# Performance work log

Measured on AMD Instinct MI355X. Metric: run time of the kernel, lower is better.

Reference implementation:

```python
import jax, jax.numpy as jnp
import numpy as np
import math

DIMS, HEAD = 1024, 16
HD = DIMS // HEAD          # 64
B, CTX = 4, 1024
MAX_ITER, THRESH = 3, 0.5  # temp=1.0 -> q temperature scaling branch is skipped (as in torch)
LOG10_21 = math.log10(1.0 + 4000.0 / 200.0)


def _freq_angles(c):
    # compute_freqs_base: 0.2*(10**linspace(0, log10(21), d/2) - 1), custom_freqs = 36000/220 * base
    d2 = HD // 2
    mel = 10.0 ** jnp.linspace(0.0, LOG10_21, d2) - 1.0
    freqs = (36000.0 / 220.0) * (200.0 * mel / 1000.0)        # [d2]
    t = jnp.arange(c, dtype=jnp.float32)
    return t[:, None] * freqs[None, :]                          # [c, d2]


def _rope(x, ang):
    # lucidrains rotary_embedding_torch convention: interleaved pairs (x0,x1),(x2,x3),...
    x1, x2 = x[..., 0::2], x[..., 1::2]
    cos, sin = jnp.cos(ang), jnp.sin(ang)
    out = jnp.stack([x1 * cos - x2 * sin, x1 * sin + x2 * cos], axis=-1)
    return out.reshape(x.shape)


def _rms(x, w):
    eps = jnp.finfo(x.dtype).eps  # torch nn.RMSNorm eps=None default
    return x * jax.lax.rsqrt(jnp.mean(jnp.square(x), -1, keepdims=True) + eps) * w


def _sdpa(q, k, v):
    # mask is always None in this module's forward -> non-causal SDPA
    s = jnp.einsum('bhqd,bhkd->bhqk', q, k) / math.sqrt(q.shape[-1])
    return jnp.einsum('bhqk,bhkd->bhqd', jax.nn.softmax(s, -1), v)


def _focus(x, xa, P):
    # x: [b, cq, D] queries, xa: [b, ck, D] keys/values. In our configs cq == ck == eff_span.
    b, cq, D = x.shape
    ck = xa.shape[1]
    q = _rms(x, P['wq_norm']) @ P['Wq'] + P['bq']
    q = q.reshape(b, cq, HEAD, HD).transpose(0, 2, 1, 3)                 # b h c d
    kv = _rms(xa, P['wkv_norm']) @ P['Wkv'] + P['bkv']
    kv = kv.reshape(b, ck, 2, HEAD, HD).transpose(2, 0, 3, 1, 4)         # kv b h c d
    k, v = kv[0], kv[1]
    q = _rope(q, _freq_angles(cq))
    k = _rope(k, _freq_angles(ck))

    e = min(cq, ck)  # static; equals cq in all call sites here
    curq, kc, vc = q, k[:, :, :e], v[:, :, :e]
    prev = jnp.zeros_like(q)
    attn_out = jnp.zeros_like(q)
    done = jnp.asarray(False)
    for it in range(MAX_ITER):
        # torch: q/k/v re-projected from current state EVERY iteration (k,v compound)
        qp = curq[:, :, :e] @ P['Wlq'] + P['blq']
        kp = kc @ P['Wlk'] + P['blk']
        vp = vc @ P['Wlv'] + P['blv']
        attn = _sdpa(_rms(qp, P['wln']), _rms(kp, P['wln']), vp)         # == iter_out since e == cq
        diff = jnp.mean(jnp.abs(attn - prev))
        stop = (diff < THRESH) & (it > 0) & (~done)
        attn_out = jnp.where(done, attn_out, attn)  # on the break iteration attn_out = iter_out
        done = done | stop
        curq = jnp.where(done, curq, curq + attn)
        prev = jnp.where(done, prev, attn)
        kc = jnp.where(done, kc, kp)
        vc = jnp.where(done, vc, vp)
    return attn_out.transpose(0, 2, 1, 3).reshape(b, cq, D)             # b c (h d)


def _slide(x, P):
    # win_size = head_dim; only the first win_size keys of each span are ever used
    b, ctx, D = x.shape
    w = HD
    off = w // HEAD                       # span_len - win_size
    nwin = ctx // w                       # ctx chosen as a multiple of w
    starts = jnp.maximum(jnp.arange(nwin) * w - off, 0)
    kidx = starts[:, None] + jnp.arange(w)[None, :]                      # [nwin, w]
    qwin = x.reshape(b, nwin, w, D).transpose(1, 0, 2, 3)                # [nwin, b, w, D]
    kwin = x[:, kidx, :].transpose(1, 0, 2, 3)                           # [nwin, b, w, D]
    outw = jax.vmap(lambda xq, xk: _focus(xq, xk, P))(qwin, kwin)
    return outw.transpose(1, 0, 2, 3).reshape(b, ctx, D)


def _forward(x, xa, P):
    xw = _slide(x, P)
    xaw = _slide(xa, P)
    out = _focus(xw, xaw, P)
    return out @ P['Wo'] + P['bo']        # Dropout(0.01) is identity in eval


def setup_inputs() -> dict:
    key = jax.random.key(0)
    ks = jax.random.split(key, 8)
    s = 0.02
    f32 = jnp.float32
    return {
        'x': jax.random.normal(ks[0], (B, CTX, DIMS), f32),
        'xa': jax.random.normal(ks[1], (B, CTX, DIMS), f32),
        'wq_norm': jnp.ones((DIMS,), f32),
        'Wq': jax.random.normal(ks[2], (DIMS, DIMS), f32) * s,
        'bq': jnp.zeros((DIMS,), f32),
        'wkv_norm': jnp.ones((DIMS,), f32),
        'Wkv': jax.random.normal(ks[3], (DIMS, 2 * DIMS), f32) * s,
        'bkv': jnp.zeros((2 * DIMS,), f32),
        'wln': jnp.ones((HD,), f32),
        'Wlq': jax.random.normal(ks[4], (HD, HD), f32) * s,
        'blq': jnp.zeros((HD,), f32),
        'Wlk': jax.random.normal(ks[5], (HD, HD), f32) * s,
        'blk': jnp.zeros((HD,), f32),
        'Wlv': jax.random.normal(ks[6], (HD, HD), f32) * s,
        'blv': jnp.zeros((HD,), f32),
        'Wo': jax.random.normal(ks[7], (DIMS, DIMS), f32) * s,
        'bo': jnp.zeros((DIMS,), f32),
    }


def reference(x, xa, wq_norm, Wq, bq, wkv_norm, Wkv, bkv, wln, Wlq, blq, Wlk, blk, Wlv, blv, Wo, bo):
    P = dict(wq_norm=wq_norm, Wq=Wq, bq=bq, wkv_norm=wkv_norm, Wkv=Wkv, bkv=bkv, wln=wln,
             Wlq=Wlq, blq=blq, Wlk=Wlk, blk=blk, Wlv=Wlv, blv=blv, Wo=Wo, bo=bo)
    return _forward(x, xa, P)
```

## Files before the change

### kernel.cpp

```cpp
#include <hip/hip_runtime.h>
#include <math.h>

#define TPB 256

static __device__ __forceinline__ float4 mk4(float a, float b, float c, float d) {
  float4 r; r.x = a; r.y = b; r.z = c; r.w = d; return r;
}

static __device__ __forceinline__ float4 ld4s(const float* buf, int row, int ch) {
  return *(const float4*)&buf[(row << 6) + (((ch ^ (row >> 2)) & 15) << 2)];
}
static __device__ __forceinline__ void st4s(float* buf, int row, int ch, float4 v) {
  *(float4*)&buf[(row << 6) + (((ch ^ (row >> 2)) & 15) << 2)] = v;
}

__global__ __launch_bounds__(TPB) void k_tables(float* __restrict__ cosb,
                                                float* __restrict__ sinb) {
  int gid = blockIdx.x * TPB + threadIdx.x;
  if (gid >= 1024 * 32) return;
  int t = gid >> 5, j = gid & 31;
  const double Ld = 1.3222192947339193;
  float Lf = (float)Ld;
  float mlog;
  if (j == 31) {
    mlog = Lf;
  } else {
    float stepf = (float)((double)j / 31.0);
    mlog = (float)((double)Lf * (double)stepf);
  }
  float p = (float)pow(10.0, (double)mlog);
  float mel = p - 1.0f;
  float t2 = (200.0f * mel) / 1000.0f;
  float freq = 163.63636363636363f * t2;
  float ang = (float)t * freq;
  double a = (double)ang;
  cosb[gid] = (float)cos(a);
  sinb[gid] = (float)sin(a);
}

__global__ __launch_bounds__(TPB) void k_rowinv(const float* __restrict__ X,
                                                float* __restrict__ inv) {
  __shared__ float red[4];
  int row = blockIdx.x;
  int tid = threadIdx.x;
  float4 v = *(const float4*)(X + (size_t)row * 1024 + tid * 4);
  float ss = v.x * v.x + v.y * v.y + v.z * v.z + v.w * v.w;
#pragma unroll
  for (int m = 1; m < 64; m <<= 1) ss += __shfl_xor(ss, m);
  if ((tid & 63) == 0) red[tid >> 6] = ss;
  __syncthreads();
  if (tid == 0) {
    float s = ((red[0] + red[1]) + (red[2] + red[3]));
    float mm = s * (1.0f / 1024.0f) + 1.1920928955078125e-7f;
    inv[row] = (float)(1.0 / sqrt((double)mm));
  }
}

__global__ __launch_bounds__(TPB) void k_gemm128(
    const float* __restrict__ X, const float* __restrict__ inv,
    const float* __restrict__ wn, const float* __restrict__ W,
    const float* __restrict__ bias, float* __restrict__ o0,
    float* __restrict__ o1, int N, int mode) {
  __shared__ float As[16][132];
  __shared__ float Bs[16][132];
  int tid = threadIdx.x;
  int bx = blockIdx.x, by = blockIdx.y;
  int tx = tid & 15, ty = tid >> 4;
  float c[8][8];
#pragma unroll
  for (int i = 0; i < 8; ++i)
#pragma unroll
    for (int j = 0; j < 8; ++j) c[i][j] = 0.0f;

  int arow = tid >> 1;
  float sA = 1.0f;
  if (inv) sA = inv[by * 128 + arow];
  const float* Xrow = X + (size_t)(by * 128 + arow) * 1024;

  for (int k0 = 0; k0 < 1024; k0 += 16) {
#pragma unroll
    for (int u = 0; u < 2; ++u) {
      int kq = ((tid & 1) * 2 + u) * 4;
      float4 a4 = *(const float4*)(Xrow + k0 + kq);
      if (wn) {
        float4 w4 = *(const float4*)(wn + k0 + kq);
        a4.x *= w4.x; a4.y *= w4.y; a4.z *= w4.z; a4.w *= w4.w;
      }
      a4.x *= sA; a4.y *= sA; a4.z *= sA; a4.w *= sA;
      As[kq + 0][arow] = a4.x;
      As[kq + 1][arow] = a4.y;
      As[kq + 2][arow] = a4.z;
      As[kq + 3][arow] = a4.w;
    }
#pragma unroll
    for (int u = 0; u < 2; ++u) {
      int kr = tid >> 4;
      int c4 = ((tid & 15) * 2 + u) * 4;
      *(float4*)&Bs[kr][c4] =
          *(const float4*)(W + (size_t)(k0 + kr) * N + bx * 128 + c4);
    }
    __syncthreads();
#pragma unroll
    for (int kk = 0; kk < 16; ++kk) {
      float4 a0 = *(const float4*)&As[kk][ty * 4];
      float4 a1 = *(const float4*)&As[kk][64 + ty * 4];
      float4 b0 = *(const float4*)&Bs[kk][tx * 4];
      float4 b1 = *(const float4*)&Bs[kk][64 + tx * 4];
      float av[8] = {a0.x, a0.y, a0.z, a0.w, a1.x, a1.y, a1.z, a1.w};
      float bv[8] = {b0.x, b0.y, b0.z, b0.w, b1.x, b1.y, b1.z, b1.w};
#pragma unroll
      for (int i = 0; i < 8; ++i)
#pragma unroll
        for (int j = 0; j < 8; ++j) c[i][j] += av[i] * bv[j];
    }
    __syncthreads();
  }

#pragma unroll
  for (int jh = 0; jh < 2; ++jh) {
    int colbase = bx * 128 + jh * 64 + tx * 4;
    float4 bb = {0.f, 0.f, 0.f, 0.f};
    if (bias) bb = *(const float4*)(bias + colbase);
#pragma unroll
    for (int ih = 0; ih < 2; ++ih) {
#pragma unroll
      for (int i2 = 0; i2 < 4; ++i2) {
        int row = by * 128 + ih * 64 + ty * 4 + i2;
        int ci = ih * 4 + i2;
        float4 o;
        o.x = c[ci][jh * 4 + 0] + bb.x;
        o.y = c[ci][jh * 4 + 1] + bb.y;
        o.z = c[ci][jh * 4 + 2] + bb.z;
        o.w = c[ci][jh * 4 + 3] + bb.w;
        if (mode == 0) {
          *(float4*)(o0 + (size_t)row * N + colbase) = o;
        } else {
          int b = row >> 10, t = row & 1023;
          float* dst = o0;
          int cc = colbase;
          if (mode == 2 && colbase >= 1024) { dst = o1; cc = colbase - 1024; }
          int ch = cc >> 6, d = cc & 63;
          *(float4*)(dst + ((size_t)((b * 16 + ch) * 1024 + t)) * 64 + d) = o;
        }
      }
    }
  }
}

__global__ __launch_bounds__(TPB) void k_rope(float* __restrict__ A, int mask,
                                              const float* __restrict__ cosb,
                                              const float* __restrict__ sinb) {
  int gid = blockIdx.x * TPB + threadIdx.x;
  int j = gid & 31;
  int row = gid >> 5;
  int t = row & 1023;
  int aidx = ((t & mask) << 5) + j;
  float cc = cosb[aidx], sn = sinb[aidx];
  size_t base = (size_t)row * 64;
  float x1 = A[base + 2 * j], x2 = A[base + 2 * j + 1];
  A[base + 2 * j] = x1 * cc - x2 * sn;
  A[base + 2 * j + 1] = x1 * sn + x2 * cc;
}

__global__ __launch_bounds__(TPB) void k_proj(
    const float* __restrict__ curq, float* __restrict__ kc,
    float* __restrict__ vc, float* __restrict__ qph, float* __restrict__ kph,
    const float* __restrict__ Wlq, const float* __restrict__ blq,
    const float* __restrict__ Wlk, const float* __restrict__ blk,
    const float* __restrict__ Wlv, const float* __restrict__ blv,
    const float* __restrict__ wln, int CQ, const int* __restrict__ flags) {
  int RT = CQ >> 4;
  int bid = blockIdx.x;
  int rt = bid % RT;
  int rest = bid / RT;
  int h = rest & 15; rest >>= 4;
  int b = rest & 3;
  int win = rest >> 2;
  if (flags && flags[win]) return;
  __shared__ float qs[16][68], ksm[16][68], vsm[16][68];
  __shared__ float Wqs[4096], Wks[4096], Wvs[4096];
  int tid = threadIdx.x;
#pragma unroll
  for (int i = 0; i < 4; ++i) {
    int f4 = (i * 256 + tid) * 4;
    *(float4*)&Wqs[f4] = *(const float4*)(Wlq + f4);
    *(float4*)&Wks[f4] = *(const float4*)(Wlk + f4);
    *(float4*)&Wvs[f4] = *(const float4*)(Wlv + f4);
  }
  int lr = tid >> 4, c4 = (tid & 15) * 4;
  int bh = b * 16 + h;
  size_t rowbase = (size_t)bh * 1024 + (size_t)win * CQ + rt * 16;
  size_t g = (rowbase + lr) * 64 + c4;
  *(float4*)&qs[lr][c4] = *(const float4*)(curq + g);
  *(float4*)&ksm[lr][c4] = *(const float4*)(kc + g);
  *(float4*)&vsm[lr][c4] = *(const float4*)(vc + g);
  __syncthreads();
  int r = tid >> 4, cg = tid & 15;
  const float eps = 1.1920928955078125e-7f;
  float4 wl4 = *(const float4*)(wln + cg * 4);
  size_t orow = (rowbase + r) * 64 + cg * 4;
  float4 acc;
  float ssum, rms;
  acc = *(const float4*)(blq + cg * 4);
#pragma unroll 8
  for (int k = 0; k < 64; ++k) {
    float xv = qs[r][k];
    float4 w4 = *(const float4*)&Wqs[k * 64 + cg * 4];
    acc.x += xv * w4.x; acc.y += xv * w4.y;
    acc.z += xv * w4.z; acc.w += xv * w4.w;
  }
  ssum = acc.x * acc.x + acc.y * acc.y + acc.z * acc.z + acc.w * acc.w;
#pragma unroll
  for (int m = 1; m < 16; m <<= 1) ssum += __shfl_xor(ssum, m);
  rms = (float)(1.0 / sqrt((double)(ssum * 0.015625f + eps)));
  {
    float4 o;
    o.x = acc.x * rms * wl4.x; o.y = acc.y * rms * wl4.y;
    o.z = acc.z * rms * wl4.z; o.w = acc.w * rms * wl4.w;
    *(float4*)(qph + orow) = o;
  }
  acc = *(const float4*)(blk + cg * 4);
#pragma unroll 8
  for (int k = 0; k < 64; ++k) {
    float xv = ksm[r][k];
    float4 w4 = *(const float4*)&Wks[k * 64 + cg * 4];
    acc.x += xv * w4.x; acc.y += xv * w4.y;
    acc.z += xv * w4.z; acc.w += xv * w4.w;
  }
  *(float4*)(kc + orow) = acc;
  ssum = acc.x * acc.x + acc.y * acc.y + acc.z * acc.z + acc.w * acc.w;
#pragma unroll
  for (int m = 1; m < 16; m <<= 1) ssum += __shfl_xor(ssum, m);
  rms = (float)(1.0 / sqrt((double)(ssum * 0.015625f + eps)));
  {
    float4 o;
    o.x = acc.x * rms * wl4.x; o.y = acc.y * rms * wl4.y;
    o.z = acc.z * rms * wl4.z; o.w = acc.w * rms * wl4.w;
    *(float4*)(kph + orow) = o;
  }
  acc = *(const float4*)(blv + cg * 4);
#pragma unroll 8
  for (int k = 0; k < 64; ++k) {
    float xv = vsm[r][k];
    float4 w4 = *(const float4*)&Wvs[k * 64 + cg * 4];
    acc.x += xv * w4.x; acc.y += xv * w4.y;
    acc.z += xv * w4.z; acc.w += xv * w4.w;
  }
  *(float4*)(vc + orow) = acc;
}

static __device__ __forceinline__ void slide_proj_one(
    float* src, float* rawdst, float* ndst, const float* __restrict__ W,
    const float* __restrict__ bias, float4 wl4, int tx, int ty) {
  const float eps = 1.1920928955078125e-7f;
  float4 bb = *(const float4*)(bias + tx * 4);
  float4 acc[4];
#pragma unroll
  for (int i = 0; i < 4; ++i) acc[i] = bb;
#pragma unroll 2
  for (int k4 = 0; k4 < 16; ++k4) {
    const float* w = W + (k4 * 4) * 64 + tx * 4;
    float4 w0 = *(const float4*)(w);
    float4 w1 = *(const float4*)(w + 64);
    float4 w2 = *(const float4*)(w + 128);
    float4 w3 = *(const float4*)(w + 192);
#pragma unroll
    for (int i = 0; i < 4; ++i) {
      float4 a4 = ld4s(src, ty * 4 + i, k4);
      acc[i].x += a4.x * w0.x; acc[i].y += a4.x * w0.y;
      acc[i].z += a4.x * w0.z; acc[i].w += a4.x * w0.w;
      acc[i].x += a4.y * w1.x; acc[i].y += a4.y * w1.y;
      acc[i].z += a4.y * w1.z; acc[i].w += a4.y * w1.w;
      acc[i].x += a4.z * w2.x; acc[i].y += a4.z * w2.y;
      acc[i].z += a4.z * w2.z; acc[i].w += a4.z * w2.w;
      acc[i].x += a4.w * w3.x; acc[i].y += a4.w * w3.y;
      acc[i].z += a4.w * w3.z; acc[i].w += a4.w * w3.w;
    }
  }
#pragma unroll
  for (int i = 0; i < 4; ++i) {
    int row = ty * 4 + i;
    if (rawdst) st4s(rawdst, row, tx, acc[i]);
    if (ndst) {
      float ssum = acc[i].x * acc[i].x + acc[i].y * acc[i].y +
                   acc[i].z * acc[i].z + acc[i].w * acc[i].w;
#pragma unroll
      for (int mm = 1; mm < 16; mm <<= 1) ssum += __shfl_xor(ssum, mm);
      float rms = (float)(1.0 / sqrt((double)(ssum * 0.015625f + eps)));
      st4s(ndst, row, tx, mk4(acc[i].x * rms * wl4.x, acc[i].y * rms * wl4.y,
                              acc[i].z * rms * wl4.z, acc[i].w * rms * wl4.w));
    }
  }
}

__global__ __launch_bounds__(TPB) void k_slide(
    const float* __restrict__ Qg, const float* __restrict__ Kg,
    const float* __restrict__ Vg, float* __restrict__ curqg,
    float* __restrict__ kcg, float* __restrict__ vcg, float* __restrict__ outb,
    float* __restrict__ diffp, const int* __restrict__ flags,
    const float* __restrict__ cosb, const float* __restrict__ sinb,
    const float* __restrict__ Wlq, const float* __restrict__ blq,
    const float* __restrict__ Wlk, const float* __restrict__ blk,
    const float* __restrict__ Wlv, const float* __restrict__ blv,
    const float* __restrict__ wln, int mode) {
  int bid = blockIdx.x;
  int win = bid & 15, bh = bid >> 4;
  int h = bh & 15, b = bh >> 4;
  if (mode == 2 && flags[win]) return;
  __shared__ float sX[4096], sKc[4096], sVc[4096], sQp[4096], sKp[4096];
  int tid = threadIdx.x;
  int tx = tid & 15, ty = tid >> 4;
  size_t bh1024 = (size_t)bh * 1024;
  int t0 = win * 64;
  const float SCL = 0.18033688011112042f;

  if (mode == 0) {
    int sw = (win == 0) ? 0 : win * 64 - 4;
#pragma unroll
    for (int u = 0; u < 4; ++u) {
      int f4 = u * 256 + tid;
      int row = f4 >> 4, ch = f4 & 15;
      int aidx = (row << 5) + ch * 2;
      float c0 = cosb[aidx], s0 = sinb[aidx];
      float c1 = cosb[aidx + 1], s1 = sinb[aidx + 1];
      float4 q = *(const float4*)(Qg + (bh1024 + t0 + row) * 64 + ch * 4);
      st4s(sX, row, ch, mk4(q.x * c0 - q.y * s0, q.x * s0 + q.y * c0,
                            q.z * c1 - q.w * s1, q.z * s1 + q.w * c1));
      float4 k = *(const float4*)(Kg + (bh1024 + sw + row) * 64 + ch * 4);
      st4s(sKc, row, ch, mk4(k.x * c0 - k.y * s0, k.x * s0 + k.y * c0,
                             k.z * c1 - k.w * s1, k.z * s1 + k.w * c1));
      st4s(sVc, row, ch,
           *(const float4*)(Vg + (bh1024 + sw + row) * 64 + ch * 4));
    }
  } else {
#pragma unroll
    for (int u = 0; u < 4; ++u) {
      int f4 = u * 256 + tid;
      int row = f4 >> 4, ch = f4 & 15;
      size_t g = (bh1024 + t0 + row) * 64 + ch * 4;
      st4s(sX, row, ch, *(const float4*)(curqg + g));
      st4s(sKc, row, ch, *(const float4*)(kcg + g));
      st4s(sVc, row, ch, *(const float4*)(vcg + g));
    }
  }
  float4 wl4 = *(const float4*)(wln + tx * 4);
  float4 prev4[4];
  int niter = (mode == 0) ? 2 : 1;
  for (int it = 0; it < niter; ++it) {
    __syncthreads();
    slide_proj_one(sX, nullptr, sQp, Wlq, blq, wl4, tx, ty);
    slide_proj_one(sKc, sKc, sKp, Wlk, blk, wl4, tx, ty);
    slide_proj_one(sVc, sVc, nullptr, Wlv, blv, wl4, tx, ty);
    __syncthreads();
    float s4[4][4];
#pragma unroll
    for (int i = 0; i < 4; ++i)
      s4[i][0] = s4[i][1] = s4[i][2] = s4[i][3] = 0.0f;
#pragma unroll 4
    for (int d4 = 0; d4 < 16; ++d4) {
      float4 kv[4];
#pragma unroll
      for (int j = 0; j < 4; ++j) kv[j] = ld4s(sKp, tx * 4 + j, d4);
#pragma unroll
      for (int i = 0; i < 4; ++i) {
        float4 q4 = ld4s(sQp, ty * 4 + i, d4);
#pragma unroll
        for (int j = 0; j < 4; ++j) {
          s4[i][j] += q4.x * kv[j].x;
          s4[i][j] += q4.y * kv[j].y;
          s4[i][j] += q4.z * kv[j].z;
          s4[i][j] += q4.w * kv[j].w;
        }
      }
    }
    float lrow[4];
#pragma unroll
    for (int i = 0; i < 4; ++i) {
      s4[i][0] *= SCL; s4[i][1] *= SCL; s4[i][2] *= SCL; s4[i][3] *= SCL;
      float r0 = fmaxf(fmaxf(s4[i][0], s4[i][1]), fmaxf(s4[i][2], s4[i][3]));
#pragma unroll
      for (int mm = 1; mm < 16; mm <<= 1) r0 = fmaxf(r0, __shfl_xor(r0, mm));
      float rs = 0.0f;
#pragma unroll
      for (int j = 0; j < 4; ++j) {
        float pv = exp2f(s4[i][j] - r0);
        s4[i][j] = pv;
        rs += pv;
      }
#pragma unroll
      for (int mm = 1; mm < 16; mm <<= 1) rs += __shfl_xor(rs, mm);
      lrow[i] = rs;
    }
#pragma unroll
    for (int i = 0; i < 4; ++i)
      st4s(sQp, ty * 4 + i, tx, mk4(s4[i][0], s4[i][1], s4[i][2], s4[i][3]));
    float4 av[4];
#pragma unroll
    for (int i = 0; i < 4; ++i) av[i] = mk4(0.f, 0.f, 0.f, 0.f);
#pragma unroll 4
    for (int k4 = 0; k4 < 16; ++k4) {
      float4 v4[4];
#pragma unroll
      for (int kk = 0; kk < 4; ++kk) v4[kk] = ld4s(sVc, k4 * 4 + kk, tx);
#pragma unroll
      for (int i = 0; i < 4; ++i) {
        float4 p4 = ld4s(sQp, ty * 4 + i, k4);
        av[i].x += p4.x * v4[0].x; av[i].y += p4.x * v4[0].y;
        av[i].z += p4.x * v4[0].z; av[i].w += p4.x * v4[0].w;
        av[i].x += p4.y * v4[1].x; av[i].y += p4.y * v4[1].y;
        av[i].z += p4.y * v4[1].z; av[i].w += p4.y * v4[1].w;
        av[i].x += p4.z * v4[2].x; av[i].y += p4.z * v4[2].y;
        av[i].z += p4.z * v4[2].z; av[i].w += p4.z * v4[2].w;
        av[i].x += p4.w * v4[3].x; av[i].y += p4.w * v4[3].y;
        av[i].z += p4.w * v4[3].z; av[i].w += p4.w * v4[3].w;
      }
    }
#pragma unroll
    for (int i = 0; i < 4; ++i) {
      av[i].x /= lrow[i]; av[i].y /= lrow[i];
      av[i].z /= lrow[i]; av[i].w /= lrow[i];
    }
    if (mode == 0 && it == 0) {
#pragma unroll
      for (int i = 0; i < 4; ++i) {
        prev4[i] = av[i];
        int row = ty * 4 + i;
        float4 cq = ld4s(sX, row, tx);
        cq.x += av[i].x; cq.y += av[i].y; cq.z += av[i].z; cq.w += av[i].w;
        st4s(sX, row, tx, cq);
      }
    } else if (mode == 0) {
      float ds = 0.0f;
#pragma unroll
      for (int i = 0; i < 4; ++i) {
        int row = ty * 4 + i;
        ds += fabsf(av[i].x - prev4[i].x) + fabsf(av[i].y - prev4[i].y) +
              fabsf(av[i].z - prev4[i].z) + fabsf(av[i].w - prev4[i].w);
        float4 cq = ld4s(sX, row, tx);
        cq.x += av[i].x; cq.y += av[i].y; cq.z += av[i].z; cq.w += av[i].w;
        st4s(sX, row, tx, cq);
        size_t g = (bh1024 + t0 + row) * 64 + tx * 4;
        *(float4*)(curqg + g) = cq;
        *(float4*)(kcg + g) = ld4s(sKc, row, tx);
        *(float4*)(vcg + g) = ld4s(sVc, row, tx);
        size_t obase = ((size_t)b * 1024 + t0 + row) * 1024 + h * 64 + tx * 4;
        *(float4*)(outb + obase) = av[i];
      }
      __syncthreads();
      float* red = sKp;
      red[tid] = ds;
      __syncthreads();
      for (int s2 = 128; s2 > 0; s2 >>= 1) {
        if (tid < s2) red[tid] += red[tid + s2];
        __syncthreads();
      }
      if (tid == 0) diffp[bid] = red[0];
    } else {
#pragma unroll
      for (int i = 0; i < 4; ++i) {
        int row = ty * 4 + i;
        size_t obase = ((size_t)b * 1024 + t0 + row) * 1024 + h * 64 + tx * 4;
        *(float4*)(outb + obase) = av[i];
      }
    }
  }
}

__global__ __launch_bounds__(TPB) void k_attn4(
    const float* __restrict__ qph, const float* __restrict__ kph,
    const float* __restrict__ vbuf, float* __restrict__ curq,
    float* __restrict__ prevb, float* __restrict__ outb,
    float* __restrict__ diffp, const int* __restrict__ flags, int NQT, int nt,
    int mode) {
  int bid = blockIdx.x;
  int qt = bid % NQT;
  int bh = bid / NQT;
  int h = bh & 15, b = bh >> 4;
  if (mode == 2 && flags[0]) return;
  __shared__ float sP[128 * 128];
  int tid = threadIdx.x;
  int tx = tid & 15, ty = tid >> 4;
  size_t bh1024 = (size_t)bh * 1024;
  int q0 = qt * 128;
  const float* Qb = qph + (bh1024 + q0 + ty * 8) * 64;

  float m[8], l[8], acc[8][4];
#pragma unroll
  for (int i = 0; i < 8; ++i) {
    m[i] = -INFINITY; l[i] = 0.0f;
    acc[i][0] = acc[i][1] = acc[i][2] = acc[i][3] = 0.0f;
  }
  const float SCL = 0.18033688011112042f;

  for (int kt = 0; kt < nt; ++kt) {
    int k0 = kt * 128;
    const float* Kb = kph + (bh1024 + k0 + tx * 8) * 64;
    const float* Vb = vbuf + (bh1024 + k0) * 64 + tx * 4;
    float s[8][8];
#pragma unroll
    for (int i = 0; i < 8; ++i)
#pragma unroll
      for (int j = 0; j < 8; ++j) s[i][j] = 0.0f;
#pragma unroll 4
    for (int d4 = 0; d4 < 16; ++d4) {
      float4 kv[8];
#pragma unroll
      for (int j = 0; j < 8; ++j)
        kv[j] = *(const float4*)(Kb + j * 64 + d4 * 4);
#pragma unroll
      for (int i = 0; i < 8; ++i) {
        float4 q4 = *(const float4*)(Qb + i * 64 + d4 * 4);
#pragma unroll
        for (int j = 0; j < 8; ++j) {
          s[i][j] += q4.x * kv[j].x;
          s[i][j] += q4.y * kv[j].y;
          s[i][j] += q4.z * kv[j].z;
          s[i][j] += q4.w * kv[j].w;
        }
      }
    }
#pragma unroll
    for (int i = 0; i < 8; ++i) {
#pragma unroll
      for (int j = 0; j < 8; ++j) s[i][j] *= SCL;
      float r0 = s[i][0];
#pragma unroll
      for (int j = 1; j < 8; ++j) r0 = fmaxf(r0, s[i][j]);
#pragma unroll
      for (int mm = 1; mm < 16; mm <<= 1) r0 = fmaxf(r0, __shfl_xor(r0, mm));
      float mnew = fmaxf(m[i], r0);
      float sc = exp2f(m[i] - mnew);
      float rs = 0.0f;
#pragma unroll
      for (int j = 0; j < 8; ++j) {
        float pv = exp2f(s[i][j] - mnew);
        s[i][j] = pv;
        rs += pv;
      }
#pragma unroll
      for (int mm = 1; mm < 16; mm <<= 1) rs += __shfl_xor(rs, mm);
      l[i] = l[i] * sc + rs;
      m[i] = mnew;
      acc[i][0] *= sc; acc[i][1] *= sc; acc[i][2] *= sc; acc[i][3] *= sc;
    }
#pragma unroll
    for (int i = 0; i < 8; ++i) {
      int q = ty * 8 + i;
      *(float4*)&sP[(q << 7) + ((((2 * tx) ^ ty) & 31) << 2)] =
          mk4(s[i][0], s[i][1], s[i][2], s[i][3]);
      *(float4*)&sP[(q << 7) + ((((2 * tx + 1) ^ ty) & 31) << 2)] =
          mk4(s[i][4], s[i][5], s[i][6], s[i][7]);
    }
#pragma unroll 2
    for (int k4 = 0; k4 < 32; ++k4) {
      float4 v4[4];
#pragma unroll
      for (int kk = 0; kk < 4; ++kk)
        v4[kk] = *(const float4*)(Vb + (k4 * 4 + kk) * 64);
#pragma unroll
      for (int i = 0; i < 8; ++i) {
        float4 p4 = *(const float4*)&sP[((ty * 8 + i) << 7) +
                                        (((k4 ^ ty) & 31) << 2)];
        acc[i][0] += p4.x * v4[0].x; acc[i][1] += p4.x * v4[0].y;
        acc[i][2] += p4.x * v4[0].z; acc[i][3] += p4.x * v4[0].w;
        acc[i][0] += p4.y * v4[1].x; acc[i][1] += p4.y * v4[1].y;
        acc[i][2] += p4.y * v4[1].z; acc[i][3] += p4.y * v4[1].w;
        acc[i][0] += p4.z * v4[2].x; acc[i][1] += p4.z * v4[2].y;
        acc[i][2] += p4.z * v4[2].z; acc[i][3] += p4.z * v4[2].w;
        acc[i][0] += p4.w * v4[3].x; acc[i][1] += p4.w * v4[3].y;
        acc[i][2] += p4.w * v4[3].z; acc[i][3] += p4.w * v4[3].w;
      }
    }
  }
  float ds = 0.0f;
#pragma unroll
  for (int i = 0; i < 8; ++i) {
    int t = q0 + ty * 8 + i;
    float4 att;
    att.x = acc[i][0] / l[i];
    att.y = acc[i][1] / l[i];
    att.z = acc[i][2] / l[i];
    att.w = acc[i][3] / l[i];
    size_t base = (bh1024 + t) * 64 + tx * 4;
    size_t obase = ((size_t)b * 1024 + t) * 1024 + h * 64 + tx * 4;
    if (mode == 0) {
      *(float4*)(prevb + base) = att;
      float4 cq = *(const float4*)(curq + base);
      cq.x += att.x; cq.y += att.y; cq.z += att.z; cq.w += att.w;
      *(float4*)(curq + base) = cq;
    } else if (mode == 1) {
      float4 pv = *(const float4*)(prevb + base);
      ds += fabsf(att.x - pv.x) + fabsf(att.y - pv.y) +
            fabsf(att.z - pv.z) + fabsf(att.w - pv.w);
      float4 cq = *(const float4*)(curq + base);
      cq.x += att.x; cq.y += att.y; cq.z += att.z; cq.w += att.w;
      *(float4*)(curq + base) = cq;
      *(float4*)(outb + obase) = att;
    } else {
      *(float4*)(outb + obase) = att;
    }
  }
  if (mode == 1) {
    __syncthreads();
    float* red = sP;
    red[tid] = ds;
    __syncthreads();
    for (int s2 = 128; s2 > 0; s2 >>= 1) {
      if (tid < s2) red[tid] += red[tid + s2];
      __syncthreads();
    }
    if (tid == 0) diffp[bid] = red[0];
  }
}

__global__ __launch_bounds__(64) void k_finalize(const float* __restrict__ diffp,
                                                 int* __restrict__ flags,
                                                 int nwin, int nper,
                                                 float count) {
  int w = threadIdx.x;
  if (w < nwin) {
    float s = 0.0f;
    for (int i = 0; i < nper; ++i) s += diffp[w + i * nwin];
    flags[w] = (s / count < 0.5f) ? 1 : 0;
  }
}

extern "C" void kernel_launch(void* const* d_in, const int* in_sizes, int n_in,
                              void* d_out, int out_size, void* d_ws,
                              size_t ws_size, hipStream_t stream) {
  const float* x = (const float*)d_in[0];
  const float* xa = (const float*)d_in[1];
  const float* wqn = (const float*)d_in[2];
  const float* Wq = (const float*)d_in[3];
  const float* bq = (const float*)d_in[4];
  const float* wkvn = (const float*)d_in[5];
  const float* Wkv = (const float*)d_in[6];
  const float* bkv = (const float*)d_in[7];
  const float* wln = (const float*)d_in[8];
  const float* Wlq = (const float*)d_in[9];
  const float* blq = (const float*)d_in[10];
  const float* Wlk = (const float*)d_in[11];
  const float* blk = (const float*)d_in[12];
  const float* Wlv = (const float*)d_in[13];
  const float* blv = (const float*)d_in[14];
  const float* Wo = (const float*)d_in[15];
  const float* bo = (const float*)d_in[16];

  float* ws = (float*)d_ws;
  const size_t SLOT = (size_t)4 * 16 * 1024 * 64;
  float* xw = ws;
  float* xaw = ws + SLOT;
  float* Q = ws + 2 * SLOT;
  float* K = ws + 3 * SLOT;
  float* V = ws + 4 * SLOT;
  float* kc = ws + 5 * SLOT;
  float* vc = ws + 6 * SLOT;
  float* prev = ws + 7 * SLOT;
  float* qph = ws + 8 * SLOT;
  float* kph = ws + 9 * SLOT;
  float* misc = ws + 10 * SLOT;
  float* inv = misc;
  float* cosb = misc + 8192;
  float* sinb = cosb + 32768;
  float* diffp = sinb + 32768;
  int* flags = (int*)(diffp + 4096);

  k_tables<<<128, TPB, 0, stream>>>(cosb, sinb);

  for (int sl = 0; sl < 2; ++sl) {
    const float* Xin = sl ? xa : x;
    float* Xout = sl ? xaw : xw;
    k_rowinv<<<4096, TPB, 0, stream>>>(Xin, inv);
    k_gemm128<<<dim3(8, 32), TPB, 0, stream>>>(Xin, inv, wqn, Wq, bq, Q, nullptr, 1024, 1);
    k_gemm128<<<dim3(16, 32), TPB, 0, stream>>>(Xin, inv, wkvn, Wkv, bkv, K, V, 2048, 2);
    k_slide<<<1024, TPB, 0, stream>>>(Q, K, V, Q, kc, vc, Xout, diffp, nullptr,
                                      cosb, sinb, Wlq, blq, Wlk, blk, Wlv, blv,
                                      wln, 0);
    k_finalize<<<1, 64, 0, stream>>>(diffp, flags, 16, 64, 262144.0f);
    k_slide<<<1024, TPB, 0, stream>>>(Q, K, V, Q, kc, vc, Xout, diffp, flags,
                                      cosb, sinb, Wlq, blq, Wlk, blk, Wlv, blv,
                                      wln, 2);
  }

  k_rowinv<<<4096, TPB, 0, stream>>>(xw, inv);
  k_gemm128<<<dim3(8, 32), TPB, 0, stream>>>(xw, inv, wqn, Wq, bq, Q, nullptr, 1024, 1);
  k_rowinv<<<4096, TPB, 0, stream>>>(xaw, inv);
  k_gemm128<<<dim3(16, 32), TPB, 0, stream>>>(xaw, inv, wkvn, Wkv, bkv, K, V, 2048, 2);
  k_rope<<<8192, TPB, 0, stream>>>(Q, 1023, cosb, sinb);
  k_rope<<<8192, TPB, 0, stream>>>(K, 1023, cosb, sinb);
  float* fout = xw;
  k_proj<<<4096, TPB, 0, stream>>>(Q, K, V, qph, kph, Wlq, blq, Wlk, blk, Wlv, blv, wln, 1024, nullptr);
  k_attn4<<<512, TPB, 0, stream>>>(qph, kph, V, Q, prev, fout, diffp, nullptr, 8, 8, 0);
  k_proj<<<4096, TPB, 0, stream>>>(Q, K, V, qph, kph, Wlq, blq, Wlk, blk, Wlv, blv, wln, 1024, nullptr);
  k_attn4<<<512, TPB, 0, stream>>>(qph, kph, V, Q, prev, fout, diffp, nullptr, 8, 8, 1);
  k_finalize<<<1, 64, 0, stream>>>(diffp, flags, 1, 512, 4194304.0f);
  k_proj<<<4096, TPB, 0, stream>>>(Q, K, V, qph, kph, Wlq, blq, Wlk, blk, Wlv, blv, wln, 1024, flags);
  k_attn4<<<512, TPB, 0, stream>>>(qph, kph, V, Q, prev, fout, diffp, flags, 8, 8, 2);

  k_gemm128<<<dim3(8, 32), TPB, 0, stream>>>(fout, nullptr, nullptr, Wo, bo, (float*)d_out, nullptr, 1024, 0);
}
```

Baseline: 2.869 ms.

## Store normalized keys transposed and shrink attention key tile to 64

```diff
diff --git a/kernel.cpp b/kernel.cpp
--- a/kernel.cpp
+++ b/kernel.cpp
@@ -164,7 +164,7 @@
 
 __global__ __launch_bounds__(TPB) void k_proj(
     const float* __restrict__ curq, float* __restrict__ kc,
-    float* __restrict__ vc, float* __restrict__ qph, float* __restrict__ kph,
+    float* __restrict__ vc, float* __restrict__ qph, float* __restrict__ kphT,
     const float* __restrict__ Wlq, const float* __restrict__ blq,
     const float* __restrict__ Wlk, const float* __restrict__ blk,
     const float* __restrict__ Wlv, const float* __restrict__ blv,
@@ -196,6 +196,7 @@
   *(float4*)&vsm[lr][c4] = *(const float4*)(vc + g);
   __syncthreads();
   int r = tid >> 4, cg = tid & 15;
+  int tglob = win * CQ + rt * 16 + r;
   const float eps = 1.1920928955078125e-7f;
   float4 wl4 = *(const float4*)(wln + cg * 4);
   size_t orow = (rowbase + r) * 64 + cg * 4;
@@ -233,10 +234,15 @@
   for (int m = 1; m < 16; m <<= 1) ssum += __shfl_xor(ssum, m);
   rms = (float)(1.0 / sqrt((double)(ssum * 0.015625f + eps)));
   {
-    float4 o;
-    o.x = acc.x * rms * wl4.x; o.y = acc.y * rms * wl4.y;
-    o.z = acc.z * rms * wl4.z; o.w = acc.w * rms * wl4.w;
-    *(float4*)(kph + orow) = o;
+    float no0 = acc.x * rms * wl4.x;
+    float no1 = acc.y * rms * wl4.y;
+    float no2 = acc.z * rms * wl4.z;
+    float no3 = acc.w * rms * wl4.w;
+    size_t tb = (size_t)bh * 64 + cg * 4;
+    kphT[(tb + 0) * 1024 + tglob] = no0;
+    kphT[(tb + 1) * 1024 + tglob] = no1;
+    kphT[(tb + 2) * 1024 + tglob] = no2;
+    kphT[(tb + 3) * 1024 + tglob] = no3;
   }
   acc = *(const float4*)(blv + cg * 4);
 #pragma unroll 8
@@ -466,8 +472,8 @@
   }
 }
 
-__global__ __launch_bounds__(TPB) void k_attn4(
-    const float* __restrict__ qph, const float* __restrict__ kph,
+__global__ __launch_bounds__(TPB) void k_attn5(
+    const float* __restrict__ qph, const float* __restrict__ kphT,
     const float* __restrict__ vbuf, float* __restrict__ curq,
     float* __restrict__ prevb, float* __restrict__ outb,
     float* __restrict__ diffp, const int* __restrict__ flags, int NQT, int nt,
@@ -477,10 +483,11 @@
   int bh = bid / NQT;
   int h = bh & 15, b = bh >> 4;
   if (mode == 2 && flags[0]) return;
-  __shared__ float sP[128 * 128];
+  __shared__ float sP[128 * 64];
   int tid = threadIdx.x;
   int tx = tid & 15, ty = tid >> 4;
   size_t bh1024 = (size_t)bh * 1024;
+  size_t bh64 = (size_t)bh * 64;
   int q0 = qt * 128;
   const float* Qb = qph + (bh1024 + q0 + ty * 8) * 64;
 
@@ -493,46 +500,46 @@
   const float SCL = 0.18033688011112042f;
 
   for (int kt = 0; kt < nt; ++kt) {
-    int k0 = kt * 128;
-    const float* Kb = kph + (bh1024 + k0 + tx * 8) * 64;
+    int k0 = kt * 64;
+    const float* KTb = kphT + bh64 * 1024 + k0 + tx * 4;
     const float* Vb = vbuf + (bh1024 + k0) * 64 + tx * 4;
-    float s[8][8];
+    float s[8][4];
 #pragma unroll
     for (int i = 0; i < 8; ++i)
-#pragma unroll
-      for (int j = 0; j < 8; ++j) s[i][j] = 0.0f;
+      s[i][0] = s[i][1] = s[i][2] = s[i][3] = 0.0f;
 #pragma unroll 4
     for (int d4 = 0; d4 < 16; ++d4) {
-      float4 kv[8];
-#pragma unroll
-      for (int j = 0; j < 8; ++j)
-        kv[j] = *(const float4*)(Kb + j * 64 + d4 * 4);
+      float4 kv[4];
+#pragma unroll
+      for (int dd = 0; dd < 4; ++dd)
+        kv[dd] = *(const float4*)(KTb + (size_t)(d4 * 4 + dd) * 1024);
 #pragma unroll
       for (int i = 0; i < 8; ++i) {
         float4 q4 = *(const float4*)(Qb + i * 64 + d4 * 4);
 #pragma unroll
-        for (int j = 0; j < 8; ++j) {
-          s[i][j] += q4.x * kv[j].x;
-          s[i][j] += q4.y * kv[j].y;
-          s[i][j] += q4.z * kv[j].z;
-          s[i][j] += q4.w * kv[j].w;
+        for (int j = 0; j < 4; ++j) {
+          float kj0 = (j == 0) ? kv[0].x : (j == 1) ? kv[0].y : (j == 2) ? kv[0].z : kv[0].w;
+          float kj1 = (j == 0) ? kv[1].x : (j == 1) ? kv[1].y : (j == 2) ? kv[1].z : kv[1].w;
+          float kj2 = (j == 0) ? kv[2].x : (j == 1) ? kv[2].y : (j == 2) ? kv[2].z : kv[2].w;
+          float kj3 = (j == 0) ? kv[3].x : (j == 1) ? kv[3].y : (j == 2) ? kv[3].z : kv[3].w;
+          s[i][j] += q4.x * kj0;
+          s[i][j] += q4.y * kj1;
+          s[i][j] += q4.z * kj2;
+          s[i][j] += q4.w * kj3;
         }
       }
     }
 #pragma unroll
     for (int i = 0; i < 8; ++i) {
-#pragma unroll
-      for (int j = 0; j < 8; ++j) s[i][j] *= SCL;
-      float r0 = s[i][0];
-#pragma unroll
-      for (int j = 1; j < 8; ++j) r0 = fmaxf(r0, s[i][j]);
+      s[i][0] *= SCL; s[i][1] *= SCL; s[i][2] *= SCL; s[i][3] *= SCL;
+      float r0 = fmaxf(fmaxf(s[i][0], s[i][1]), fmaxf(s[i][2], s[i][3]));
 #pragma unroll
       for (int mm = 1; mm < 16; mm <<= 1) r0 = fmaxf(r0, __shfl_xor(r0, mm));
       float mnew = fmaxf(m[i], r0);
       float sc = exp2f(m[i] - mnew);
       float rs = 0.0f;
 #pragma unroll
-      for (int j = 0; j < 8; ++j) {
+      for (int j = 0; j < 4; ++j) {
         float pv = exp2f(s[i][j] - mnew);
         s[i][j] = pv;
         rs += pv;
@@ -546,21 +553,20 @@
 #pragma unroll
     for (int i = 0; i < 8; ++i) {
       int q = ty * 8 + i;
-      *(float4*)&sP[(q << 7) + ((((2 * tx) ^ ty) & 31) << 2)] =
+      *(float4*)&sP[(q << 6) + (((tx ^ (q >> 3)) & 15) << 2)] =
           mk4(s[i][0], s[i][1], s[i][2], s[i][3]);
-      *(float4*)&sP[(q << 7) + ((((2 * tx + 1) ^ ty) & 31) << 2)] =
-          mk4(s[i][4], s[i][5], s[i][6], s[i][7]);
-    }
-#pragma unroll 2
-    for (int k4 = 0; k4 < 32; ++k4) {
+    }
+#pragma unroll 4
+    for (int k4 = 0; k4 < 16; ++k4) {
       float4 v4[4];
 #pragma unroll
       for (int kk = 0; kk < 4; ++kk)
         v4[kk] = *(const float4*)(Vb + (k4 * 4 + kk) * 64);
 #pragma unroll
       for (int i = 0; i < 8; ++i) {
-        float4 p4 = *(const float4*)&sP[((ty * 8 + i) << 7) +
-                                        (((k4 ^ ty) & 31) << 2)];
+        int q = ty * 8 + i;
+        float4 p4 = *(const float4*)&sP[(q << 6) +
+                                        (((k4 ^ (q >> 3)) & 15) << 2)];
         acc[i][0] += p4.x * v4[0].x; acc[i][1] += p4.x * v4[0].y;
         acc[i][2] += p4.x * v4[0].z; acc[i][3] += p4.x * v4[0].w;
         acc[i][0] += p4.y * v4[1].x; acc[i][1] += p4.y * v4[1].y;
@@ -657,7 +663,7 @@
   float* vc = ws + 6 * SLOT;
   float* prev = ws + 7 * SLOT;
   float* qph = ws + 8 * SLOT;
-  float* kph = ws + 9 * SLOT;
+  float* kphT = ws + 9 * SLOT;
   float* misc = ws + 10 * SLOT;
   float* inv = misc;
   float* cosb = misc + 8192;
@@ -689,13 +695,13 @@
   k_rope<<<8192, TPB, 0, stream>>>(Q, 1023, cosb, sinb);
   k_rope<<<8192, TPB, 0, stream>>>(K, 1023, cosb, sinb);
   float* fout = xw;
-  k_proj<<<4096, TPB, 0, stream>>>(Q, K, V, qph, kph, Wlq, blq, Wlk, blk, Wlv, blv, wln, 1024, nullptr);
-  k_attn4<<<512, TPB, 0, stream>>>(qph, kph, V, Q, prev, fout, diffp, nullptr, 8, 8, 0);
-  k_proj<<<4096, TPB, 0, stream>>>(Q, K, V, qph, kph, Wlq, blq, Wlk, blk, Wlv, blv, wln, 1024, nullptr);
-  k_attn4<<<512, TPB, 0, stream>>>(qph, kph, V, Q, prev, fout, diffp, nullptr, 8, 8, 1);
+  k_proj<<<4096, TPB, 0, stream>>>(Q, K, V, qph, kphT, Wlq, blq, Wlk, blk, Wlv, blv, wln, 1024, nullptr);
+  k_attn5<<<512, TPB, 0, stream>>>(qph, kphT, V, Q, prev, fout, diffp, nullptr, 8, 16, 0);
+  k_proj<<<4096, TPB, 0, stream>>>(Q, K, V, qph, kphT, Wlq, blq, Wlk, blk, Wlv, blv, wln, 1024, nullptr);
+  k_attn5<<<512, TPB, 0, stream>>>(qph, kphT, V, Q, prev, fout, diffp, nullptr, 8, 16, 1);
   k_finalize<<<1, 64, 0, stream>>>(diffp, flags, 1, 512, 4194304.0f);
-  k_proj<<<4096, TPB, 0, stream>>>(Q, K, V, qph, kph, Wlq, blq, Wlk, blk, Wlv, blv, wln, 1024, flags);
-  k_attn4<<<512, TPB, 0, stream>>>(qph, kph, V, Q, prev, fout, diffp, flags, 8, 8, 2);
+  k_proj<<<4096, TPB, 0, stream>>>(Q, K, V, qph, kphT, Wlq, blq, Wlk, blk, Wlv, blv, wln, 1024, flags);
+  k_attn5<<<512, TPB, 0, stream>>>(qph, kphT, V, Q, prev, fout, diffp, flags, 8, 16, 2);
 
   k_gemm128<<<dim3(8, 32), TPB, 0, stream>>>(fout, nullptr, nullptr, Wo, bo, (float*)d_out, nullptr, 1024, 0);
 }
```

After: 2.523 ms. 12.0% less time.

## Stage K/V tiles in shared memory for attention and read GEMM weights directly

Applied to the files above, without the earlier changes.

```diff
diff --git a/kernel.cpp b/kernel.cpp
--- a/kernel.cpp
+++ b/kernel.cpp
@@ -56,26 +56,28 @@
   }
 }
 
-__global__ __launch_bounds__(TPB) void k_gemm128(
+template <int BN>
+__global__ __launch_bounds__(TPB) void k_gemm(
     const float* __restrict__ X, const float* __restrict__ inv,
     const float* __restrict__ wn, const float* __restrict__ W,
     const float* __restrict__ bias, float* __restrict__ o0,
     float* __restrict__ o1, int N, int mode) {
+  constexpr int JW = BN / 64;
   __shared__ float As[16][132];
-  __shared__ float Bs[16][132];
   int tid = threadIdx.x;
   int bx = blockIdx.x, by = blockIdx.y;
   int tx = tid & 15, ty = tid >> 4;
-  float c[8][8];
+  float c[8][4 * JW];
 #pragma unroll
   for (int i = 0; i < 8; ++i)
 #pragma unroll
-    for (int j = 0; j < 8; ++j) c[i][j] = 0.0f;
+    for (int j = 0; j < 4 * JW; ++j) c[i][j] = 0.0f;
 
   int arow = tid >> 1;
   float sA = 1.0f;
   if (inv) sA = inv[by * 128 + arow];
   const float* Xrow = X + (size_t)(by * 128 + arow) * 1024;
+  const float* Wb = W + bx * BN + tx * 4;
 
   for (int k0 = 0; k0 < 1024; k0 += 16) {
 #pragma unroll
@@ -92,33 +94,31 @@
       As[kq + 2][arow] = a4.z;
       As[kq + 3][arow] = a4.w;
     }
-#pragma unroll
-    for (int u = 0; u < 2; ++u) {
-      int kr = tid >> 4;
-      int c4 = ((tid & 15) * 2 + u) * 4;
-      *(float4*)&Bs[kr][c4] =
-          *(const float4*)(W + (size_t)(k0 + kr) * N + bx * 128 + c4);
-    }
     __syncthreads();
 #pragma unroll
     for (int kk = 0; kk < 16; ++kk) {
       float4 a0 = *(const float4*)&As[kk][ty * 4];
       float4 a1 = *(const float4*)&As[kk][64 + ty * 4];
-      float4 b0 = *(const float4*)&Bs[kk][tx * 4];
-      float4 b1 = *(const float4*)&Bs[kk][64 + tx * 4];
       float av[8] = {a0.x, a0.y, a0.z, a0.w, a1.x, a1.y, a1.z, a1.w};
-      float bv[8] = {b0.x, b0.y, b0.z, b0.w, b1.x, b1.y, b1.z, b1.w};
+      const float* wrow = Wb + (size_t)(k0 + kk) * N;
+      float4 b0 = *(const float4*)(wrow);
+      float bv[4 * JW];
+      bv[0] = b0.x; bv[1] = b0.y; bv[2] = b0.z; bv[3] = b0.w;
+      if (JW == 2) {
+        float4 b1 = *(const float4*)(wrow + 64);
+        bv[4] = b1.x; bv[5] = b1.y; bv[6] = b1.z; bv[7] = b1.w;
+      }
 #pragma unroll
       for (int i = 0; i < 8; ++i)
 #pragma unroll
-        for (int j = 0; j < 8; ++j) c[i][j] += av[i] * bv[j];
+        for (int j = 0; j < 4 * JW; ++j) c[i][j] += av[i] * bv[j];
     }
     __syncthreads();
   }
 
 #pragma unroll
-  for (int jh = 0; jh < 2; ++jh) {
-    int colbase = bx * 128 + jh * 64 + tx * 4;
+  for (int jh = 0; jh < JW; ++jh) {
+    int colbase = bx * BN + jh * 64 + tx * 4;
     float4 bb = {0.f, 0.f, 0.f, 0.f};
     if (bias) bb = *(const float4*)(bias + colbase);
 #pragma unroll
@@ -466,7 +466,7 @@
   }
 }
 
-__global__ __launch_bounds__(TPB) void k_attn4(
+__global__ __launch_bounds__(TPB) void k_attn6(
     const float* __restrict__ qph, const float* __restrict__ kph,
     const float* __restrict__ vbuf, float* __restrict__ curq,
     float* __restrict__ prevb, float* __restrict__ outb,
@@ -477,7 +477,9 @@
   int bh = bid / NQT;
   int h = bh & 15, b = bh >> 4;
   if (mode == 2 && flags[0]) return;
-  __shared__ float sP[128 * 128];
+  __shared__ float sK[4096];
+  __shared__ float sV[4096];
+  __shared__ float sP[8192];
   int tid = threadIdx.x;
   int tx = tid & 15, ty = tid >> 4;
   size_t bh1024 = (size_t)bh * 1024;
@@ -493,25 +495,31 @@
   const float SCL = 0.18033688011112042f;
 
   for (int kt = 0; kt < nt; ++kt) {
-    int k0 = kt * 128;
-    const float* Kb = kph + (bh1024 + k0 + tx * 8) * 64;
-    const float* Vb = vbuf + (bh1024 + k0) * 64 + tx * 4;
-    float s[8][8];
+    int k0 = kt * 64;
+#pragma unroll
+    for (int u = 0; u < 4; ++u) {
+      int f4 = u * 256 + tid;
+      int row = f4 >> 4, ch = f4 & 15;
+      st4s(sK, row, ch,
+           *(const float4*)(kph + (bh1024 + k0 + row) * 64 + ch * 4));
+      st4s(sV, row, ch,
+           *(const float4*)(vbuf + (bh1024 + k0 + row) * 64 + ch * 4));
+    }
+    __syncthreads();
+    float s[8][4];
 #pragma unroll
     for (int i = 0; i < 8; ++i)
-#pragma unroll
-      for (int j = 0; j < 8; ++j) s[i][j] = 0.0f;
+      s[i][0] = s[i][1] = s[i][2] = s[i][3] = 0.0f;
 #pragma unroll 4
     for (int d4 = 0; d4 < 16; ++d4) {
-      float4 kv[8];
-#pragma unroll
-      for (int j = 0; j < 8; ++j)
-        kv[j] = *(const float4*)(Kb + j * 64 + d4 * 4);
+      float4 kv[4];
+#pragma unroll
+      for (int j = 0; j < 4; ++j) kv[j] = ld4s(sK, tx * 4 + j, d4);
 #pragma unroll
       for (int i = 0; i < 8; ++i) {
         float4 q4 = *(const float4*)(Qb + i * 64 + d4 * 4);
 #pragma unroll
-        for (int j = 0; j < 8; ++j) {
+        for (int j = 0; j < 4; ++j) {
           s[i][j] += q4.x * kv[j].x;
           s[i][j] += q4.y * kv[j].y;
           s[i][j] += q4.z * kv[j].z;
@@ -521,18 +529,15 @@
     }
 #pragma unroll
     for (int i = 0; i < 8; ++i) {
-#pragma unroll
-      for (int j = 0; j < 8; ++j) s[i][j] *= SCL;
-      float r0 = s[i][0];
-#pragma unroll
-      for (int j = 1; j < 8; ++j) r0 = fmaxf(r0, s[i][j]);
+      s[i][0] *= SCL; s[i][1] *= SCL; s[i][2] *= SCL; s[i][3] *= SCL;
+      float r0 = fmaxf(fmaxf(s[i][0], s[i][1]), fmaxf(s[i][2], s[i][3]));
 #pragma unroll
       for (int mm = 1; mm < 16; mm <<= 1) r0 = fmaxf(r0, __shfl_xor(r0, mm));
       float mnew = fmaxf(m[i], r0);
       float sc = exp2f(m[i] - mnew);
       float rs = 0.0f;
 #pragma unroll
-      for (int j = 0; j < 8; ++j) {
+      for (int j = 0; j < 4; ++j) {
         float pv = exp2f(s[i][j] - mnew);
         s[i][j] = pv;
         rs += pv;
@@ -546,21 +551,19 @@
 #pragma unroll
     for (int i = 0; i < 8; ++i) {
       int q = ty * 8 + i;
-      *(float4*)&sP[(q << 7) + ((((2 * tx) ^ ty) & 31) << 2)] =
+      *(float4*)&sP[(q << 6) + (((tx ^ (q >> 3)) & 15) << 2)] =
           mk4(s[i][0], s[i][1], s[i][2], s[i][3]);
-      *(float4*)&sP[(q << 7) + ((((2 * tx + 1) ^ ty) & 31) << 2)] =
-          mk4(s[i][4], s[i][5], s[i][6], s[i][7]);
-    }
-#pragma unroll 2
-    for (int k4 = 0; k4 < 32; ++k4) {
+    }
+#pragma unroll 4
+    for (int k4 = 0; k4 < 16; ++k4) {
       float4 v4[4];
 #pragma unroll
-      for (int kk = 0; kk < 4; ++kk)
-        v4[kk] = *(const float4*)(Vb + (k4 * 4 + kk) * 64);
+      for (int kk = 0; kk < 4; ++kk) v4[kk] = ld4s(sV, k4 * 4 + kk, tx);
 #pragma unroll
       for (int i = 0; i < 8; ++i) {
-        float4 p4 = *(const float4*)&sP[((ty * 8 + i) << 7) +
-                                        (((k4 ^ ty) & 31) << 2)];
+        int q = ty * 8 + i;
+        float4 p4 = *(const float4*)&sP[(q << 6) +
+                                        (((k4 ^ (q >> 3)) & 15) << 2)];
         acc[i][0] += p4.x * v4[0].x; acc[i][1] += p4.x * v4[0].y;
         acc[i][2] += p4.x * v4[0].z; acc[i][3] += p4.x * v4[0].w;
         acc[i][0] += p4.y * v4[1].x; acc[i][1] += p4.y * v4[1].y;
@@ -571,6 +574,7 @@
         acc[i][2] += p4.w * v4[3].z; acc[i][3] += p4.w * v4[3].w;
       }
     }
+    __syncthreads();
   }
   float ds = 0.0f;
 #pragma unroll
@@ -671,8 +675,8 @@
     const float* Xin = sl ? xa : x;
     float* Xout = sl ? xaw : xw;
     k_rowinv<<<4096, TPB, 0, stream>>>(Xin, inv);
-    k_gemm128<<<dim3(8, 32), TPB, 0, stream>>>(Xin, inv, wqn, Wq, bq, Q, nullptr, 1024, 1);
-    k_gemm128<<<dim3(16, 32), TPB, 0, stream>>>(Xin, inv, wkvn, Wkv, bkv, K, V, 2048, 2);
+    k_gemm<64><<<dim3(16, 32), TPB, 0, stream>>>(Xin, inv, wqn, Wq, bq, Q, nullptr, 1024, 1);
+    k_gemm<128><<<dim3(16, 32), TPB, 0, stream>>>(Xin, inv, wkvn, Wkv, bkv, K, V, 2048, 2);
     k_slide<<<1024, TPB, 0, stream>>>(Q, K, V, Q, kc, vc, Xout, diffp, nullptr,
                                       cosb, sinb, Wlq, blq, Wlk, blk, Wlv, blv,
                                       wln, 0);
@@ -683,19 +687,19 @@
   }
 
   k_rowinv<<<4096, TPB, 0, stream>>>(xw, inv);
-  k_gemm128<<<dim3(8, 32), TPB, 0, stream>>>(xw, inv, wqn, Wq, bq, Q, nullptr, 1024, 1);
+  k_gemm<64><<<dim3(16, 32), TPB, 0, stream>>>(xw, inv, wqn, Wq, bq, Q, nullptr, 1024, 1);
   k_rowinv<<<4096, TPB, 0, stream>>>(xaw, inv);
-  k_gemm128<<<dim3(16, 32), TPB, 0, stream>>>(xaw, inv, wkvn, Wkv, bkv, K, V, 2048, 2);
+  k_gemm<128><<<dim3(16, 32), TPB, 0, stream>>>(xaw, inv, wkvn, Wkv, bkv, K, V, 2048, 2);
   k_rope<<<8192, TPB, 0, stream>>>(Q, 1023, cosb, sinb);
   k_rope<<<8192, TPB, 0, stream>>>(K, 1023, cosb, sinb);
   float* fout = xw;
   k_proj<<<4096, TPB, 0, stream>>>(Q, K, V, qph, kph, Wlq, blq, Wlk, blk, Wlv, blv, wln, 1024, nullptr);
-  k_attn4<<<512, TPB, 0, stream>>>(qph, kph, V, Q, prev, fout, diffp, nullptr, 8, 8, 0);
+  k_attn6<<<512, TPB, 0, stream>>>(qph, kph, V, Q, prev, fout, diffp, nullptr, 8, 16, 0);
   k_proj<<<4096, TPB, 0, stream>>>(Q, K, V, qph, kph, Wlq, blq, Wlk, blk, Wlv, blv, wln, 1024, nullptr);
-  k_attn4<<<512, TPB, 0, stream>>>(qph, kph, V, Q, prev, fout, diffp, nullptr, 8, 8, 1);
+  k_attn6<<<512, TPB, 0, stream>>>(qph, kph, V, Q, prev, fout, diffp, nullptr, 8, 16, 1);
   k_finalize<<<1, 64, 0, stream>>>(diffp, flags, 1, 512, 4194304.0f);
   k_proj<<<4096, TPB, 0, stream>>>(Q, K, V, qph, kph, Wlq, blq, Wlk, blk, Wlv, blv, wln, 1024, flags);
-  k_attn4<<<512, TPB, 0, stream>>>(qph, kph, V, Q, prev, fout, diffp, flags, 8, 8, 2);
-
-  k_gemm128<<<dim3(8, 32), TPB, 0, stream>>>(fout, nullptr, nullptr, Wo, bo, (float*)d_out, nullptr, 1024, 0);
-}
+  k_attn6<<<512, TPB, 0, stream>>>(qph, kph, V, Q, prev, fout, diffp, flags, 8, 16, 2);
+
+  k_gemm<64><<<dim3(16, 32), TPB, 0, stream>>>(fout, nullptr, nullptr, Wo, bo, (float*)d_out, nullptr, 1024, 0);
+}
```

Result: faster. 2.467 ms (-14.0%).
